# Kernel tuning notes

Hardware: AMD Instinct MI355X
Metric: run time of the kernel (lower is better)

## Reference

```python
import jax, jax.numpy as jnp
import numpy as np

B, S, H = 2, 256, 512
EPS = 1e-12  # TPLinker conditional LayerNorm default epsilon
NEG = -1e30  # finite stand-in for -inf in running max


def _cond_layer_norm(x, cond, Wg, Wb, gamma, beta):
    # TPLinker conditional LayerNorm: gamma/beta are modulated by a linear map of cond.
    g = gamma + cond @ Wg          # (..., H)
    b = beta + cond @ Wb           # (..., H)
    xc = x - jnp.mean(x, axis=-1, keepdims=True)
    inv = jax.lax.rsqrt(jnp.mean(xc * xc, axis=-1, keepdims=True) + EPS)
    return xc * inv * g + b


def setup_inputs() -> dict:
    key = jax.random.key(0)
    ks = jax.random.split(key, 6)
    return {
        "seq_hiddens": jax.random.normal(ks[0], (B, S, H), jnp.float32),
        "mask": jnp.ones((B, S), jnp.float32),
        "lamtha": jax.random.uniform(ks[1], (H,), jnp.float32),
        "Wg1": jax.random.normal(ks[2], (H, H), jnp.float32) * 0.02,
        "Wb1": jax.random.normal(ks[3], (H, H), jnp.float32) * 0.02,
        "g1": jnp.ones((H,), jnp.float32),
        "b1": jnp.zeros((H,), jnp.float32),
        "Wg2": jax.random.normal(ks[4], (H, H), jnp.float32) * 0.02,
        "Wb2": jax.random.normal(ks[5], (H, H), jnp.float32) * 0.02,
        "g2": jnp.ones((H,), jnp.float32),
        "b2": jnp.zeros((H,), jnp.float32),
    }


def reference(seq_hiddens, mask, lamtha, Wg1, Wb1, g1, b1, Wg2, Wb2, g2, b2):
    # mask additive penalty, broadcast over hidden (matches (1-mask)*-1000 expand)
    seq = seq_hiddens + ((1.0 - mask) * -1000.0)[:, :, None]  # (B,S,H)

    ii, jj = jnp.triu_indices(S)  # row-major pairs (i, j>=i), same order as the torch loop

    # window means over seq[i..j] via cumulative sums (replaces O(S^3) recomputation)
    csum = jnp.cumsum(seq, axis=1)                              # (B,S,H)
    lens = (jj - ii + 1).astype(seq.dtype)[None, :, None]
    mean_pairs = (csum[:, jj] - csum[:, ii] + seq[:, ii]) / lens  # (B,P,H)

    # window maxes over seq[i..j]: scan over j keeping running max per start i
    idx = jnp.arange(S)

    def step(state, j):
        sj = jnp.take(seq, j, axis=1)  # (B,H)
        new = jnp.where((idx <= j)[None, :, None],
                        jnp.maximum(state, sj[:, None, :]),
                        jnp.asarray(NEG, seq.dtype))
        return new, new

    _, Mall = jax.lax.scan(step, jnp.full((B, S, H), NEG, seq.dtype), idx)  # (S_j,B,S_i,H)
    max_pairs = Mall[jj, :, ii].transpose(1, 0, 2)  # (B,P,H)

    # mix pooling
    inner = lamtha * mean_pairs + (1.0 - lamtha) * max_pairs  # (B,P,H)

    visible = seq[:, jj]  # (B,P,H) token j
    repeat = seq[:, ii]   # (B,P,H) token i

    shaking = _cond_layer_norm(visible, repeat, Wg1, Wb1, g1, b1)
    return _cond_layer_norm(shaking, inner, Wg2, Wb2, g2, b2)
```

## Files before the change

### kernel.cpp

```cpp
#include <hip/hip_runtime.h>
#include <hip/hip_bf16.h>

typedef __hip_bfloat16 bf16;
typedef short short8 __attribute__((ext_vector_type(8)));
typedef float floatx4 __attribute__((ext_vector_type(4)));

#define S 256
#define H 512
#define P 32896
#define NROWS 65792
#define NEGF -1e30f
#define EPSF 1e-12f

#define OFF_LN1    2129920u
#define OFF_G1     3178496u
#define OFF_B1     4227072u
#define OFF_WCAT   5275648u
#define OFF_II     6324224u
#define OFF_JJ     6390016u
#define OFF_MU2    6455808u
#define OFF_INV2   6718976u
#define OFF_INNER  6982144u

__device__ __forceinline__ void gld_lds16(const void* g, void* l) {
    __builtin_amdgcn_global_load_lds(
        (const __attribute__((address_space(1))) void*)g,
        (__attribute__((address_space(3))) void*)l, 16, 0, 0);
}

__global__ __launch_bounds__(512) void fusedA_kernel(
    const float* __restrict__ x, const float* __restrict__ mask,
    float* __restrict__ ln1,
    const float* __restrict__ Wg2, const float* __restrict__ Wb2,
    bf16* __restrict__ wcatT,
    unsigned short* __restrict__ ii, unsigned short* __restrict__ jj) {
    __shared__ float part[8][8][2];
    __shared__ float rstat[8][2];
    if (blockIdx.x < 64) {
        int b = blockIdx.x >> 5, sc = blockIdx.x & 31, h = threadIdx.x;
        int wave = h >> 6, lane = h & 63;
        int s0 = sc * 8;
        float v[8];
#pragma unroll
        for (int t = 0; t < 8; ++t) {
            int s = s0 + t;
            v[t] = x[(size_t)(b * S + s) * H + h] + (1.0f - mask[b * S + s]) * (-1000.0f);
        }
#pragma unroll
        for (int t = 0; t < 8; ++t) {
            float s = v[t], q = v[t] * v[t];
            for (int o = 1; o < 64; o <<= 1) { s += __shfl_xor(s, o); q += __shfl_xor(q, o); }
            if (lane == 0) { part[wave][t][0] = s; part[wave][t][1] = q; }
        }
        __syncthreads();
        if (h < 16) {
            int row = h >> 1, st = h & 1;
            float a = 0.0f;
#pragma unroll
            for (int w = 0; w < 8; ++w) a += part[w][row][st];
            rstat[row][st] = a;
        }
        __syncthreads();
#pragma unroll
        for (int t = 0; t < 8; ++t) {
            float m = rstat[t][0] * (1.0f / 512.0f);
            float var = rstat[t][1] * (1.0f / 512.0f) - m * m;
            var = var < 0.0f ? 0.0f : var;
            float inv = rsqrtf(var + EPSF);
            ln1[(size_t)(b * S + s0 + t) * H + h] = (v[t] - m) * inv;
        }
    } else {
        int n = blockIdx.x - 64;
        if (n < 1024) {
            int k = threadIdx.x;
            int tt = n >> 7, c = n & 127;
            int h = tt * 64 + (c & 63);
            float v = (c < 64) ? Wg2[(size_t)k * H + h] : Wb2[(size_t)k * H + h];
            wcatT[(size_t)n * H + k] = __float2bfloat16(v);
        } else {
            int p = (n - 1024) * 512 + threadIdx.x;
            if (p >= P) return;
            float disc = 513.0f * 513.0f - 8.0f * (float)p;
            int i = (int)((513.0f - sqrtf(disc)) * 0.5f);
            i = i < 0 ? 0 : (i > S - 1 ? S - 1 : i);
            while (i > 0 && (i * S - i * (i - 1) / 2) > p) --i;
            while (i < S - 1 && ((i + 1) * S - (i + 1) * i / 2) <= p) ++i;
            int off = i * S - i * (i - 1) / 2;
            ii[p] = (unsigned short)i;
            jj[p] = (unsigned short)(i + (p - off));
        }
    }
}

__global__ __launch_bounds__(256) void g1b1_kernel(
    const float* __restrict__ x, const float* __restrict__ mask,
    const float* __restrict__ Wg1, const float* __restrict__ Wb1,
    const float* __restrict__ g1, const float* __restrict__ b1,
    float* __restrict__ G1, float* __restrict__ B1) {
    __shared__ float rowbuf[4][H];
    int grp = blockIdx.x;
    int mat = blockIdx.y;
    int tid = threadIdx.x;
    int h0 = tid, h1 = tid + 256;
    int r0 = grp * 4;
#pragma unroll
    for (int r = 0; r < 4; ++r) {
        int row = r0 + r;
        float add = (1.0f - mask[row]) * (-1000.0f);
        rowbuf[r][h0] = x[(size_t)row * H + h0] + add;
        rowbuf[r][h1] = x[(size_t)row * H + h1] + add;
    }
    __syncthreads();
    const float* W = mat ? Wb1 : Wg1;
    float acc[4][2] = {{0, 0}, {0, 0}, {0, 0}, {0, 0}};
#pragma unroll 2
    for (int k4 = 0; k4 < 128; ++k4) {
        float4 a0 = ((const float4*)rowbuf[0])[k4];
        float4 a1 = ((const float4*)rowbuf[1])[k4];
        float4 a2 = ((const float4*)rowbuf[2])[k4];
        float4 a3 = ((const float4*)rowbuf[3])[k4];
        float w00 = W[(size_t)(k4 * 4 + 0) * H + h0], w01 = W[(size_t)(k4 * 4 + 0) * H + h1];
        float w10 = W[(size_t)(k4 * 4 + 1) * H + h0], w11 = W[(size_t)(k4 * 4 + 1) * H + h1];
        float w20 = W[(size_t)(k4 * 4 + 2) * H + h0], w21 = W[(size_t)(k4 * 4 + 2) * H + h1];
        float w30 = W[(size_t)(k4 * 4 + 3) * H + h0], w31 = W[(size_t)(k4 * 4 + 3) * H + h1];
        acc[0][0] += a0.x * w00 + a0.y * w10 + a0.z * w20 + a0.w * w30;
        acc[0][1] += a0.x * w01 + a0.y * w11 + a0.z * w21 + a0.w * w31;
        acc[1][0] += a1.x * w00 + a1.y * w10 + a1.z * w20 + a1.w * w30;
        acc[1][1] += a1.x * w01 + a1.y * w11 + a1.z * w21 + a1.w * w31;
        acc[2][0] += a2.x * w00 + a2.y * w10 + a2.z * w20 + a2.w * w30;
        acc[2][1] += a2.x * w01 + a2.y * w11 + a2.z * w21 + a2.w * w31;
        acc[3][0] += a3.x * w00 + a3.y * w10 + a3.z * w20 + a3.w * w30;
        acc[3][1] += a3.x * w01 + a3.y * w11 + a3.z * w21 + a3.w * w31;
    }
    float bias0 = (mat ? b1 : g1)[h0];
    float bias1 = (mat ? b1 : g1)[h1];
    float* dst = mat ? B1 : G1;
#pragma unroll
    for (int r = 0; r < 4; ++r) {
        dst[(size_t)(r0 + r) * H + h0] = acc[r][0] + bias0;
        dst[(size_t)(r0 + r) * H + h1] = acc[r][1] + bias1;
    }
}

__global__ __launch_bounds__(256) void innerstats_kernel(
    const float* __restrict__ x, const float* __restrict__ mask,
    const float* __restrict__ lamtha,
    const float* __restrict__ ln1, const float* __restrict__ G1,
    const float* __restrict__ B1,
    bf16* __restrict__ inner, float* __restrict__ mu2, float* __restrict__ inv2) {
    __shared__ float maskadd[256];
    int id = blockIdx.x;
    int kind = id & 1, sub = id >> 1;
    int t = sub & 255, b = sub >> 8;
    int i = b ? (255 - t) : t;
    int tid = threadIdx.x;
    int off = i * S - i * (i - 1) / 2;

    if (kind == 0) {
        int h2 = tid;
        maskadd[tid] = (1.0f - mask[b * S + tid]) * (-1000.0f);
        __syncthreads();
        float2 lam = ((const float2*)lamtha)[h2];
        float2 oml = {1.0f - lam.x, 1.0f - lam.y};
        const float2* xb = (const float2*)(x + (size_t)b * S * H);
        float2 mrun = {NEGF, NEGF};
        float2 srun = {0.0f, 0.0f};
        size_t base = (size_t)b * P + (size_t)off;
        __hip_bfloat162* dst = (__hip_bfloat162*)inner;
        int j = i;
#define INNER_STEP(xx, jx)                                                 \
    {                                                                      \
        float ma = maskadd[jx];                                            \
        float vx = xx.x + ma, vy = xx.y + ma;                              \
        srun.x += vx;                                                      \
        srun.y += vy;                                                      \
        mrun.x = fmaxf(mrun.x, vx);                                        \
        mrun.y = fmaxf(mrun.y, vy);                                        \
        float rl = 1.0f / (float)((jx) - i + 1);                           \
        float mx = srun.x * rl;                                            \
        float my = srun.y * rl;                                            \
        __hip_bfloat162 o;                                                 \
        o.x = __float2bfloat16(lam.x * mx + oml.x * mrun.x);               \
        o.y = __float2bfloat16(lam.y * my + oml.y * mrun.y);               \
        dst[(base + (size_t)((jx) - i)) * 256 + h2] = o;                   \
    }
        for (; j + 4 <= S; j += 4) {
            float2 x0 = xb[(j + 0) * 256 + h2];
            float2 x1 = xb[(j + 1) * 256 + h2];
            float2 x2 = xb[(j + 2) * 256 + h2];
            float2 x3 = xb[(j + 3) * 256 + h2];
            INNER_STEP(x0, j + 0)
            INNER_STEP(x1, j + 1)
            INNER_STEP(x2, j + 2)
            INNER_STEP(x3, j + 3)
        }
        for (; j < S; ++j) {
            float2 xv = xb[j * 256 + h2];
            INNER_STEP(xv, j)
        }
#undef INNER_STEP
    } else {
        int wave = tid >> 6, lane = tid & 63;
        const float4* gp = (const float4*)(G1 + (size_t)(b * S + i) * H);
        const float4* bp = (const float4*)(B1 + (size_t)(b * S + i) * H);
        float4 ga = gp[lane * 2], gb = gp[lane * 2 + 1];
        float4 ba = bp[lane * 2], bb = bp[lane * 2 + 1];
        for (int j = i + wave; j < S; j += 4) {
            const float4* lp = (const float4*)(ln1 + (size_t)(b * S + j) * H);
            float4 a0 = lp[lane * 2], a1 = lp[lane * 2 + 1];
            float v0 = a0.x * ga.x + ba.x, v1 = a0.y * ga.y + ba.y;
            float v2 = a0.z * ga.z + ba.z, v3 = a0.w * ga.w + ba.w;
            float v4 = a1.x * gb.x + bb.x, v5 = a1.y * gb.y + bb.y;
            float v6 = a1.z * gb.z + bb.z, v7 = a1.w * gb.w + bb.w;
            float sum = ((v0 + v1) + (v2 + v3)) + ((v4 + v5) + (v6 + v7));
            float ss = ((v0 * v0 + v1 * v1) + (v2 * v2 + v3 * v3)) +
                       ((v4 * v4 + v5 * v5) + (v6 * v6 + v7 * v7));
            for (int o = 1; o < 64; o <<= 1) { sum += __shfl_xor(sum, o); ss += __shfl_xor(ss, o); }
            if (lane == 0) {
                int r = b * P + off + (j - i);
                float m = sum * (1.0f / 512.0f);
                float var = ss * (1.0f / 512.0f) - m * m;
                var = var < 0.0f ? 0.0f : var;
                mu2[r] = m;
                inv2[r] = rsqrtf(var + EPSF);
            }
        }
    }
}

__global__ __launch_bounds__(256, 2) void gemm_kernel(
    const bf16* __restrict__ inner, const bf16* __restrict__ wcatT,
    const float* __restrict__ g2, const float* __restrict__ b2,
    const float* __restrict__ ln1, const float* __restrict__ G1, const float* __restrict__ B1,
    const unsigned short* __restrict__ ii, const unsigned short* __restrict__ jj,
    const float* __restrict__ mu2, const float* __restrict__ inv2,
    float* __restrict__ out) {
    extern __shared__ __align__(16) char smem[];

    const int tid = threadIdx.x;
    const int wave = tid >> 6, lane = tid & 63;
    const int q = lane >> 4, l15 = lane & 15;
    const int wm = wave & 1, wn = wave >> 1;

    const int id = blockIdx.x;
    int rb, t;
    if (id < 4096) { rb = (id >> 6) * 8 + (id & 7); t = (id >> 3) & 7; }
    else           { int w = id - 4096; rb = 512 + (w & 1); t = w >> 1; }
    const int R0 = rb * 128;

    const int srow = tid >> 3;
    const int sx8 = ((tid & 7) ^ (srow & 7)) * 8;
    const bf16* const Ag = inner + (size_t)(R0 + srow) * H + sx8;
    const bf16* const Bg = wcatT + (size_t)(t * 128 + srow) * H + sx8;

    char* const A0 = smem;
    char* const B0 = smem + 16384;
    char* const A1 = smem + 32768;
    char* const B1s = smem + 49152;

    floatx4 acc[4][4];
#pragma unroll
    for (int a = 0; a < 4; ++a)
#pragma unroll
        for (int c = 0; c < 4; ++c) acc[a][c] = (floatx4){0.f, 0.f, 0.f, 0.f};

    auto STAGE = [&](int kt, char* Ad, char* Bd) {
#pragma unroll
        for (int i2 = 0; i2 < 4; ++i2)
            gld_lds16(Ag + (size_t)i2 * 32 * H + kt * 64, Ad + i2 * 4096 + wave * 1024);
#pragma unroll
        for (int i2 = 0; i2 < 4; ++i2)
            gld_lds16(Bg + (size_t)i2 * 32 * H + kt * 64, Bd + i2 * 4096 + wave * 1024);
    };

    STAGE(0, A0, B0);
    STAGE(1, A1, B1s);
    asm volatile("s_waitcnt vmcnt(8)" ::: "memory");
    asm volatile("s_barrier" ::: "memory");

#pragma unroll
    for (int kt = 0; kt < 8; ++kt) {
        char* const As = (kt & 1) ? A1 : A0;
        char* const Bs = (kt & 1) ? B1s : B0;

        short8 bfr[4][2], af[4][2];
#pragma unroll
        for (int ks = 0; ks < 2; ++ks) {
#pragma unroll
            for (int fn = 0; fn < 4; ++fn) {
                int nr = (fn < 2 ? wn * 32 + fn * 16 : 64 + wn * 32 + (fn - 2) * 16) + l15;
                bfr[fn][ks] = *(const short8*)(Bs + nr * 128 + (((ks * 4 + q) ^ (l15 & 7)) << 4));
            }
#pragma unroll
            for (int fm = 0; fm < 4; ++fm) {
                int mr = wm * 64 + fm * 16 + l15;
                af[fm][ks] = *(const short8*)(As + mr * 128 + (((ks * 4 + q) ^ (l15 & 7)) << 4));
            }
        }

        __builtin_amdgcn_s_setprio(1);
#pragma unroll
        for (int fm = 0; fm < 4; ++fm)
#pragma unroll
            for (int fn = 0; fn < 4; ++fn)
                acc[fm][fn] = __builtin_amdgcn_mfma_f32_16x16x32_bf16(af[fm][0], bfr[fn][0], acc[fm][fn], 0, 0, 0);
        __builtin_amdgcn_s_setprio(0);

        if (kt < 6) {
            asm volatile("s_waitcnt lgkmcnt(0)" ::: "memory");
            asm volatile("s_barrier" ::: "memory");
            STAGE(kt + 2, As, Bs);
        }

        __builtin_amdgcn_s_setprio(1);
#pragma unroll
        for (int fm = 0; fm < 4; ++fm)
#pragma unroll
            for (int fn = 0; fn < 4; ++fn)
                acc[fm][fn] = __builtin_amdgcn_mfma_f32_16x16x32_bf16(af[fm][1], bfr[fn][1], acc[fm][fn], 0, 0, 0);
        __builtin_amdgcn_s_setprio(0);

        if (kt < 6) {
            asm volatile("s_waitcnt vmcnt(8)" ::: "memory");
            asm volatile("s_barrier" ::: "memory");
        } else if (kt == 6) {
            asm volatile("s_waitcnt vmcnt(0)" ::: "memory");
            asm volatile("s_barrier" ::: "memory");
        }
    }

    float g2v[2], b2v[2];
#pragma unroll
    for (int fg = 0; fg < 2; ++fg) {
        int h = t * 64 + wn * 32 + fg * 16 + l15;
        g2v[fg] = g2[h];
        b2v[fg] = b2[h];
    }
#pragma unroll
    for (int fm = 0; fm < 4; ++fm) {
#pragma unroll
        for (int r = 0; r < 4; ++r) {
            int m = wm * 64 + fm * 16 + q * 4 + r;
            int rg = R0 + m;
            int b = (rg >= P) ? 1 : 0;
            int p = rg - b * P;
            int i = ii[p], j = jj[p];
            float mu = mu2[rg], iv = inv2[rg];
            const float* lp = ln1 + (size_t)(b * S + j) * H + t * 64 + wn * 32;
            const float* gp = G1 + (size_t)(b * S + i) * H + t * 64 + wn * 32;
            const float* bp = B1 + (size_t)(b * S + i) * H + t * 64 + wn * 32;
            float* op = out + (size_t)rg * H + t * 64 + wn * 32;
#pragma unroll
            for (int fg = 0; fg < 2; ++fg) {
                int c = fg * 16 + l15;
                float s = (lp[c] * gp[c] + bp[c] - mu) * iv;
                float G2v = acc[fm][fg][r] + g2v[fg];
                float B2v = acc[fm][fg + 2][r] + b2v[fg];
                op[c] = s * G2v + B2v;
            }
        }
    }
}

extern "C" void kernel_launch(void* const* d_in, const int* in_sizes, int n_in,
                              void* d_out, int out_size, void* d_ws, size_t ws_size,
                              hipStream_t stream) {
    const float* x = (const float*)d_in[0];
    const float* mask = (const float*)d_in[1];
    const float* lamtha = (const float*)d_in[2];
    const float* Wg1 = (const float*)d_in[3];
    const float* Wb1 = (const float*)d_in[4];
    const float* g1 = (const float*)d_in[5];
    const float* b1 = (const float*)d_in[6];
    const float* Wg2 = (const float*)d_in[7];
    const float* Wb2 = (const float*)d_in[8];
    const float* g2 = (const float*)d_in[9];
    const float* b2 = (const float*)d_in[10];
    float* out = (float*)d_out;

    char* ws = (char*)d_ws;
    float* ln1 = (float*)(ws + OFF_LN1);
    float* G1 = (float*)(ws + OFF_G1);
    float* B1 = (float*)(ws + OFF_B1);
    bf16* wcatT = (bf16*)(ws + OFF_WCAT);
    unsigned short* iiA = (unsigned short*)(ws + OFF_II);
    unsigned short* jjA = (unsigned short*)(ws + OFF_JJ);
    float* mu2 = (float*)(ws + OFF_MU2);
    float* inv2 = (float*)(ws + OFF_INV2);
    bf16* inner = (bf16*)(ws + OFF_INNER);

    static bool attr_set = false;
    if (!attr_set) {
        hipFuncSetAttribute((const void*)gemm_kernel,
                            hipFuncAttributeMaxDynamicSharedMemorySize, 65536);
        attr_set = true;
    }

    hipLaunchKernelGGL(fusedA_kernel, dim3(1153), dim3(512), 0, stream,
                       x, mask, ln1, Wg2, Wb2, wcatT, iiA, jjA);
    hipLaunchKernelGGL(g1b1_kernel, dim3(128, 2), dim3(256), 0, stream,
                       x, mask, Wg1, Wb1, g1, b1, G1, B1);
    hipLaunchKernelGGL(innerstats_kernel, dim3(1024), dim3(256), 0, stream,
                       x, mask, lamtha, ln1, G1, B1, inner, mu2, inv2);
    hipLaunchKernelGGL(gemm_kernel, dim3(4112), dim3(256), 65536, stream,
                       inner, wcatT, g2, b2, ln1, G1, B1, iiA, jjA, mu2, inv2, out);
}
```

Measured before the change: 301.5 us.

## Regroup preprocessing kernels by dependency to cut launch count from four to three

The inner-pooling producer, the G1/B1 matvec, the LN1 row normalisation, the weight transpose and the index tables all become independent block ranges of one pre-kernel. The stats pass that needs ln1/G1/B1 moves to its own kernel, so one launch is removed and the independent work can run concurrently. The inner loop also reads 1/len from a shared-memory table and uses a packed bf16x2 conversion, and the matvec inner loop is unrolled over 8 k values. The risk is load imbalance inside the combined grid, since the heavy inner blocks sit alongside many light transpose blocks.

```diff
diff --git a/kernel.cpp b/kernel.cpp
--- a/kernel.cpp
+++ b/kernel.cpp
@@ -28,161 +28,51 @@
         (__attribute__((address_space(3))) void*)l, 16, 0, 0);
 }
 
-__global__ __launch_bounds__(512) void fusedA_kernel(
+__global__ __launch_bounds__(256) void pre_kernel(
     const float* __restrict__ x, const float* __restrict__ mask,
-    float* __restrict__ ln1,
-    const float* __restrict__ Wg2, const float* __restrict__ Wb2,
-    bf16* __restrict__ wcatT,
-    unsigned short* __restrict__ ii, unsigned short* __restrict__ jj) {
-    __shared__ float part[8][8][2];
-    __shared__ float rstat[8][2];
-    if (blockIdx.x < 64) {
-        int b = blockIdx.x >> 5, sc = blockIdx.x & 31, h = threadIdx.x;
-        int wave = h >> 6, lane = h & 63;
-        int s0 = sc * 8;
-        float v[8];
-#pragma unroll
-        for (int t = 0; t < 8; ++t) {
-            int s = s0 + t;
-            v[t] = x[(size_t)(b * S + s) * H + h] + (1.0f - mask[b * S + s]) * (-1000.0f);
-        }
-#pragma unroll
-        for (int t = 0; t < 8; ++t) {
-            float s = v[t], q = v[t] * v[t];
-            for (int o = 1; o < 64; o <<= 1) { s += __shfl_xor(s, o); q += __shfl_xor(q, o); }
-            if (lane == 0) { part[wave][t][0] = s; part[wave][t][1] = q; }
-        }
-        __syncthreads();
-        if (h < 16) {
-            int row = h >> 1, st = h & 1;
-            float a = 0.0f;
-#pragma unroll
-            for (int w = 0; w < 8; ++w) a += part[w][row][st];
-            rstat[row][st] = a;
-        }
-        __syncthreads();
-#pragma unroll
-        for (int t = 0; t < 8; ++t) {
-            float m = rstat[t][0] * (1.0f / 512.0f);
-            float var = rstat[t][1] * (1.0f / 512.0f) - m * m;
-            var = var < 0.0f ? 0.0f : var;
-            float inv = rsqrtf(var + EPSF);
-            ln1[(size_t)(b * S + s0 + t) * H + h] = (v[t] - m) * inv;
-        }
-    } else {
-        int n = blockIdx.x - 64;
-        if (n < 1024) {
-            int k = threadIdx.x;
-            int tt = n >> 7, c = n & 127;
-            int h = tt * 64 + (c & 63);
-            float v = (c < 64) ? Wg2[(size_t)k * H + h] : Wb2[(size_t)k * H + h];
-            wcatT[(size_t)n * H + k] = __float2bfloat16(v);
-        } else {
-            int p = (n - 1024) * 512 + threadIdx.x;
-            if (p >= P) return;
-            float disc = 513.0f * 513.0f - 8.0f * (float)p;
-            int i = (int)((513.0f - sqrtf(disc)) * 0.5f);
-            i = i < 0 ? 0 : (i > S - 1 ? S - 1 : i);
-            while (i > 0 && (i * S - i * (i - 1) / 2) > p) --i;
-            while (i < S - 1 && ((i + 1) * S - (i + 1) * i / 2) <= p) ++i;
-            int off = i * S - i * (i - 1) / 2;
-            ii[p] = (unsigned short)i;
-            jj[p] = (unsigned short)(i + (p - off));
-        }
-    }
-}
-
-__global__ __launch_bounds__(256) void g1b1_kernel(
-    const float* __restrict__ x, const float* __restrict__ mask,
+    const float* __restrict__ lamtha,
     const float* __restrict__ Wg1, const float* __restrict__ Wb1,
     const float* __restrict__ g1, const float* __restrict__ b1,
-    float* __restrict__ G1, float* __restrict__ B1) {
+    const float* __restrict__ Wg2, const float* __restrict__ Wb2,
+    float* __restrict__ ln1, float* __restrict__ G1, float* __restrict__ B1,
+    bf16* __restrict__ wcatT,
+    unsigned short* __restrict__ ii, unsigned short* __restrict__ jj,
+    bf16* __restrict__ inner) {
+    __shared__ float sh_a[256];
+    __shared__ float sh_b[256];
     __shared__ float rowbuf[4][H];
-    int grp = blockIdx.x;
-    int mat = blockIdx.y;
-    int tid = threadIdx.x;
-    int h0 = tid, h1 = tid + 256;
-    int r0 = grp * 4;
-#pragma unroll
-    for (int r = 0; r < 4; ++r) {
-        int row = r0 + r;
-        float add = (1.0f - mask[row]) * (-1000.0f);
-        rowbuf[r][h0] = x[(size_t)row * H + h0] + add;
-        rowbuf[r][h1] = x[(size_t)row * H + h1] + add;
-    }
-    __syncthreads();
-    const float* W = mat ? Wb1 : Wg1;
-    float acc[4][2] = {{0, 0}, {0, 0}, {0, 0}, {0, 0}};
-#pragma unroll 2
-    for (int k4 = 0; k4 < 128; ++k4) {
-        float4 a0 = ((const float4*)rowbuf[0])[k4];
-        float4 a1 = ((const float4*)rowbuf[1])[k4];
-        float4 a2 = ((const float4*)rowbuf[2])[k4];
-        float4 a3 = ((const float4*)rowbuf[3])[k4];
-        float w00 = W[(size_t)(k4 * 4 + 0) * H + h0], w01 = W[(size_t)(k4 * 4 + 0) * H + h1];
-        float w10 = W[(size_t)(k4 * 4 + 1) * H + h0], w11 = W[(size_t)(k4 * 4 + 1) * H + h1];
-        float w20 = W[(size_t)(k4 * 4 + 2) * H + h0], w21 = W[(size_t)(k4 * 4 + 2) * H + h1];
-        float w30 = W[(size_t)(k4 * 4 + 3) * H + h0], w31 = W[(size_t)(k4 * 4 + 3) * H + h1];
-        acc[0][0] += a0.x * w00 + a0.y * w10 + a0.z * w20 + a0.w * w30;
-        acc[0][1] += a0.x * w01 + a0.y * w11 + a0.z * w21 + a0.w * w31;
-        acc[1][0] += a1.x * w00 + a1.y * w10 + a1.z * w20 + a1.w * w30;
-        acc[1][1] += a1.x * w01 + a1.y * w11 + a1.z * w21 + a1.w * w31;
-        acc[2][0] += a2.x * w00 + a2.y * w10 + a2.z * w20 + a2.w * w30;
-        acc[2][1] += a2.x * w01 + a2.y * w11 + a2.z * w21 + a2.w * w31;
-        acc[3][0] += a3.x * w00 + a3.y * w10 + a3.z * w20 + a3.w * w30;
-        acc[3][1] += a3.x * w01 + a3.y * w11 + a3.z * w21 + a3.w * w31;
-    }
-    float bias0 = (mat ? b1 : g1)[h0];
-    float bias1 = (mat ? b1 : g1)[h1];
-    float* dst = mat ? B1 : G1;
-#pragma unroll
-    for (int r = 0; r < 4; ++r) {
-        dst[(size_t)(r0 + r) * H + h0] = acc[r][0] + bias0;
-        dst[(size_t)(r0 + r) * H + h1] = acc[r][1] + bias1;
-    }
-}
-
-__global__ __launch_bounds__(256) void innerstats_kernel(
-    const float* __restrict__ x, const float* __restrict__ mask,
-    const float* __restrict__ lamtha,
-    const float* __restrict__ ln1, const float* __restrict__ G1,
-    const float* __restrict__ B1,
-    bf16* __restrict__ inner, float* __restrict__ mu2, float* __restrict__ inv2) {
-    __shared__ float maskadd[256];
-    int id = blockIdx.x;
-    int kind = id & 1, sub = id >> 1;
-    int t = sub & 255, b = sub >> 8;
-    int i = b ? (255 - t) : t;
-    int tid = threadIdx.x;
-    int off = i * S - i * (i - 1) / 2;
-
-    if (kind == 0) {
+    __shared__ float part[4][8][2];
+    __shared__ float rstat[8][2];
+    const int id = blockIdx.x, tid = threadIdx.x;
+
+    if (id < 512) {
+        int t = id & 255, b = id >> 8;
+        int i = b ? (255 - t) : t;
+        sh_a[tid] = (1.0f - mask[b * S + tid]) * (-1000.0f);
+        sh_b[tid] = 1.0f / (float)(tid + 1);
+        __syncthreads();
         int h2 = tid;
-        maskadd[tid] = (1.0f - mask[b * S + tid]) * (-1000.0f);
-        __syncthreads();
         float2 lam = ((const float2*)lamtha)[h2];
         float2 oml = {1.0f - lam.x, 1.0f - lam.y};
         const float2* xb = (const float2*)(x + (size_t)b * S * H);
         float2 mrun = {NEGF, NEGF};
         float2 srun = {0.0f, 0.0f};
-        size_t base = (size_t)b * P + (size_t)off;
+        size_t base = (size_t)b * P + (size_t)(i * S - i * (i - 1) / 2);
         __hip_bfloat162* dst = (__hip_bfloat162*)inner;
         int j = i;
 #define INNER_STEP(xx, jx)                                                 \
     {                                                                      \
-        float ma = maskadd[jx];                                            \
+        float ma = sh_a[jx];                                               \
         float vx = xx.x + ma, vy = xx.y + ma;                              \
         srun.x += vx;                                                      \
         srun.y += vy;                                                      \
         mrun.x = fmaxf(mrun.x, vx);                                        \
         mrun.y = fmaxf(mrun.y, vy);                                        \
-        float rl = 1.0f / (float)((jx) - i + 1);                           \
-        float mx = srun.x * rl;                                            \
-        float my = srun.y * rl;                                            \
-        __hip_bfloat162 o;                                                 \
-        o.x = __float2bfloat16(lam.x * mx + oml.x * mrun.x);               \
-        o.y = __float2bfloat16(lam.y * my + oml.y * mrun.y);               \
-        dst[(base + (size_t)((jx) - i)) * 256 + h2] = o;                   \
+        float rl = sh_b[(jx) - i];                                         \
+        float fx = lam.x * (srun.x * rl) + oml.x * mrun.x;                 \
+        float fy = lam.y * (srun.y * rl) + oml.y * mrun.y;                 \
+        dst[(base + (size_t)((jx) - i)) * 256 + h2] =                      \
+            __float22bfloat162_rn(make_float2(fx, fy));                    \
     }
         for (; j + 4 <= S; j += 4) {
             float2 x0 = xb[(j + 0) * 256 + h2];
@@ -199,31 +89,145 @@
             INNER_STEP(xv, j)
         }
 #undef INNER_STEP
+    } else if (id < 768) {
+        int sub = id - 512;
+        int grp = sub >> 1, mat = sub & 1;
+        int h0 = tid, h1 = tid + 256;
+        int r0 = grp * 4;
+#pragma unroll
+        for (int r = 0; r < 4; ++r) {
+            int row = r0 + r;
+            float add = (1.0f - mask[row]) * (-1000.0f);
+            rowbuf[r][h0] = x[(size_t)row * H + h0] + add;
+            rowbuf[r][h1] = x[(size_t)row * H + h1] + add;
+        }
+        __syncthreads();
+        const float* W = mat ? Wb1 : Wg1;
+        float acc[4][2] = {{0, 0}, {0, 0}, {0, 0}, {0, 0}};
+        for (int k8 = 0; k8 < 64; ++k8) {
+            float4 ra[4][2];
+#pragma unroll
+            for (int r = 0; r < 4; ++r) {
+                ra[r][0] = ((const float4*)rowbuf[r])[k8 * 2];
+                ra[r][1] = ((const float4*)rowbuf[r])[k8 * 2 + 1];
+            }
+            float w0[8], w1[8];
+#pragma unroll
+            for (int kk = 0; kk < 8; ++kk) {
+                w0[kk] = W[(size_t)(k8 * 8 + kk) * H + h0];
+                w1[kk] = W[(size_t)(k8 * 8 + kk) * H + h1];
+            }
+#pragma unroll
+            for (int r = 0; r < 4; ++r) {
+                acc[r][0] += ra[r][0].x * w0[0] + ra[r][0].y * w0[1] +
+                             ra[r][0].z * w0[2] + ra[r][0].w * w0[3] +
+                             ra[r][1].x * w0[4] + ra[r][1].y * w0[5] +
+                             ra[r][1].z * w0[6] + ra[r][1].w * w0[7];
+                acc[r][1] += ra[r][0].x * w1[0] + ra[r][0].y * w1[1] +
+                             ra[r][0].z * w1[2] + ra[r][0].w * w1[3] +
+                             ra[r][1].x * w1[4] + ra[r][1].y * w1[5] +
+                             ra[r][1].z * w1[6] + ra[r][1].w * w1[7];
+            }
+        }
+        float bias0 = (mat ? b1 : g1)[h0];
+        float bias1 = (mat ? b1 : g1)[h1];
+        float* dst = mat ? B1 : G1;
+#pragma unroll
+        for (int r = 0; r < 4; ++r) {
+            dst[(size_t)(r0 + r) * H + h0] = acc[r][0] + bias0;
+            dst[(size_t)(r0 + r) * H + h1] = acc[r][1] + bias1;
+        }
+    } else if (id < 832) {
+        int blk = id - 768;
+        int b = blk >> 5, sc = blk & 31;
+        int s0 = sc * 8;
+        int wave = tid >> 6, lane = tid & 63;
+        int h0 = tid, h1 = tid + 256;
+        float v0[8], v1[8];
+#pragma unroll
+        for (int t = 0; t < 8; ++t) {
+            int row = b * S + s0 + t;
+            float add = (1.0f - mask[row]) * (-1000.0f);
+            v0[t] = x[(size_t)row * H + h0] + add;
+            v1[t] = x[(size_t)row * H + h1] + add;
+        }
+#pragma unroll
+        for (int t = 0; t < 8; ++t) {
+            float s = v0[t] + v1[t];
+            float q = v0[t] * v0[t] + v1[t] * v1[t];
+            for (int o = 1; o < 64; o <<= 1) { s += __shfl_xor(s, o); q += __shfl_xor(q, o); }
+            if (lane == 0) { part[wave][t][0] = s; part[wave][t][1] = q; }
+        }
+        __syncthreads();
+        if (tid < 16) {
+            int row = tid >> 1, st = tid & 1;
+            rstat[row][st] = part[0][row][st] + part[1][row][st] +
+                             part[2][row][st] + part[3][row][st];
+        }
+        __syncthreads();
+#pragma unroll
+        for (int t = 0; t < 8; ++t) {
+            float m = rstat[t][0] * (1.0f / 512.0f);
+            float var = rstat[t][1] * (1.0f / 512.0f) - m * m;
+            var = var < 0.0f ? 0.0f : var;
+            float inv = rsqrtf(var + EPSF);
+            int row = b * S + s0 + t;
+            ln1[(size_t)row * H + h0] = (v0[t] - m) * inv;
+            ln1[(size_t)row * H + h1] = (v1[t] - m) * inv;
+        }
+    } else if (id < 1856) {
+        int n = id - 832;
+        int tt = n >> 7, c = n & 127;
+        int h = tt * 64 + (c & 63);
+        const float* Wsrc = (c < 64) ? Wg2 : Wb2;
+        int k0 = tid, k1 = tid + 256;
+        wcatT[(size_t)n * H + k0] = __float2bfloat16(Wsrc[(size_t)k0 * H + h]);
+        wcatT[(size_t)n * H + k1] = __float2bfloat16(Wsrc[(size_t)k1 * H + h]);
     } else {
-        int wave = tid >> 6, lane = tid & 63;
-        const float4* gp = (const float4*)(G1 + (size_t)(b * S + i) * H);
-        const float4* bp = (const float4*)(B1 + (size_t)(b * S + i) * H);
-        float4 ga = gp[lane * 2], gb = gp[lane * 2 + 1];
-        float4 ba = bp[lane * 2], bb = bp[lane * 2 + 1];
-        for (int j = i + wave; j < S; j += 4) {
-            const float4* lp = (const float4*)(ln1 + (size_t)(b * S + j) * H);
-            float4 a0 = lp[lane * 2], a1 = lp[lane * 2 + 1];
-            float v0 = a0.x * ga.x + ba.x, v1 = a0.y * ga.y + ba.y;
-            float v2 = a0.z * ga.z + ba.z, v3 = a0.w * ga.w + ba.w;
-            float v4 = a1.x * gb.x + bb.x, v5 = a1.y * gb.y + bb.y;
-            float v6 = a1.z * gb.z + bb.z, v7 = a1.w * gb.w + bb.w;
-            float sum = ((v0 + v1) + (v2 + v3)) + ((v4 + v5) + (v6 + v7));
-            float ss = ((v0 * v0 + v1 * v1) + (v2 * v2 + v3 * v3)) +
-                       ((v4 * v4 + v5 * v5) + (v6 * v6 + v7 * v7));
-            for (int o = 1; o < 64; o <<= 1) { sum += __shfl_xor(sum, o); ss += __shfl_xor(ss, o); }
-            if (lane == 0) {
-                int r = b * P + off + (j - i);
-                float m = sum * (1.0f / 512.0f);
-                float var = ss * (1.0f / 512.0f) - m * m;
-                var = var < 0.0f ? 0.0f : var;
-                mu2[r] = m;
-                inv2[r] = rsqrtf(var + EPSF);
-            }
+        int p = (id - 1856) * 256 + tid;
+        if (p >= P) return;
+        float disc = 513.0f * 513.0f - 8.0f * (float)p;
+        int i = (int)((513.0f - sqrtf(disc)) * 0.5f);
+        i = i < 0 ? 0 : (i > S - 1 ? S - 1 : i);
+        while (i > 0 && (i * S - i * (i - 1) / 2) > p) --i;
+        while (i < S - 1 && ((i + 1) * S - (i + 1) * i / 2) <= p) ++i;
+        int off = i * S - i * (i - 1) / 2;
+        ii[p] = (unsigned short)i;
+        jj[p] = (unsigned short)(i + (p - off));
+    }
+}
+
+__global__ __launch_bounds__(256) void stats_kernel(
+    const float* __restrict__ ln1, const float* __restrict__ G1,
+    const float* __restrict__ B1,
+    float* __restrict__ mu2, float* __restrict__ inv2) {
+    int id = blockIdx.x;
+    int t = id & 255, b = id >> 8;
+    int i = b ? (255 - t) : t;
+    int tid = threadIdx.x, wave = tid >> 6, lane = tid & 63;
+    int off = i * S - i * (i - 1) / 2;
+    const float4* gp = (const float4*)(G1 + (size_t)(b * S + i) * H);
+    const float4* bp = (const float4*)(B1 + (size_t)(b * S + i) * H);
+    float4 ga = gp[lane * 2], gb = gp[lane * 2 + 1];
+    float4 ba = bp[lane * 2], bb = bp[lane * 2 + 1];
+    for (int j = i + wave; j < S; j += 4) {
+        const float4* lp = (const float4*)(ln1 + (size_t)(b * S + j) * H);
+        float4 a0 = lp[lane * 2], a1 = lp[lane * 2 + 1];
+        float v0 = a0.x * ga.x + ba.x, v1 = a0.y * ga.y + ba.y;
+        float v2 = a0.z * ga.z + ba.z, v3 = a0.w * ga.w + ba.w;
+        float v4 = a1.x * gb.x + bb.x, v5 = a1.y * gb.y + bb.y;
+        float v6 = a1.z * gb.z + bb.z, v7 = a1.w * gb.w + bb.w;
+        float sum = ((v0 + v1) + (v2 + v3)) + ((v4 + v5) + (v6 + v7));
+        float ss = ((v0 * v0 + v1 * v1) + (v2 * v2 + v3 * v3)) +
+                   ((v4 * v4 + v5 * v5) + (v6 * v6 + v7 * v7));
+        for (int o = 1; o < 64; o <<= 1) { sum += __shfl_xor(sum, o); ss += __shfl_xor(ss, o); }
+        if (lane == 0) {
+            int r = b * P + off + (j - i);
+            float m = sum * (1.0f / 512.0f);
+            float var = ss * (1.0f / 512.0f) - m * m;
+            var = var < 0.0f ? 0.0f : var;
+            mu2[r] = m;
+            inv2[r] = rsqrtf(var + EPSF);
         }
     }
 }
@@ -396,12 +400,11 @@
         attr_set = true;
     }
 
-    hipLaunchKernelGGL(fusedA_kernel, dim3(1153), dim3(512), 0, stream,
-                       x, mask, ln1, Wg2, Wb2, wcatT, iiA, jjA);
-    hipLaunchKernelGGL(g1b1_kernel, dim3(128, 2), dim3(256), 0, stream,
-                       x, mask, Wg1, Wb1, g1, b1, G1, B1);
-    hipLaunchKernelGGL(innerstats_kernel, dim3(1024), dim3(256), 0, stream,
-                       x, mask, lamtha, ln1, G1, B1, inner, mu2, inv2);
+    hipLaunchKernelGGL(pre_kernel, dim3(1985), dim3(256), 0, stream,
+                       x, mask, lamtha, Wg1, Wb1, g1, b1, Wg2, Wb2,
+                       ln1, G1, B1, wcatT, iiA, jjA, inner);
+    hipLaunchKernelGGL(stats_kernel, dim3(512), dim3(256), 0, stream,
+                       ln1, G1, B1, mu2, inv2);
     hipLaunchKernelGGL(gemm_kernel, dim3(4112), dim3(256), 65536, stream,
                        inner, wcatT, g2, b2, ln1, G1, B1, iiA, jjA, mu2, inv2, out);
 }
```

Measured after the change: 307.6 us. +2.0%, slower.

## Retile GEMM to 256-row blocks with K=32 stages and regroup weight layout

Applied to the files above, without the earlier changes.

The main GEMM now uses 256x128 output tiles instead of 128x128, with half-width K stages (32 elements) and a new swizzled LDS layout. The weight transpose is reordered so each wave's G/B columns sit together. The aim is to halve the number of blocks and re-reads of the weight tile, raising MFMA work per LDS load. It doubles accumulator registers (8x4 floatx4), which risks occupancy under launch_bounds(256,2). Smaller edits unroll the g1b1 K loop by 8 and replace the per-step reciprocal in innerstats with an LDS lookup table plus a packed bf16 convert.

```diff
diff --git a/kernel.cpp b/kernel.cpp
--- a/kernel.cpp
+++ b/kernel.cpp
@@ -73,10 +73,11 @@
         int n = blockIdx.x - 64;
         if (n < 1024) {
             int k = threadIdx.x;
-            int tt = n >> 7, c = n & 127;
-            int h = tt * 64 + (c & 63);
-            float v = (c < 64) ? Wg2[(size_t)k * H + h] : Wb2[(size_t)k * H + h];
-            wcatT[(size_t)n * H + k] = __float2bfloat16(v);
+            int tt = n >> 7, u = n & 127;
+            int wnn = u >> 6, v = u & 63;
+            int h = tt * 64 + wnn * 32 + (v & 31);
+            float val = (v < 32) ? Wg2[(size_t)k * H + h] : Wb2[(size_t)k * H + h];
+            wcatT[(size_t)n * H + k] = __float2bfloat16(val);
         } else {
             int p = (n - 1024) * 512 + threadIdx.x;
             if (p >= P) return;
@@ -113,24 +114,30 @@
     __syncthreads();
     const float* W = mat ? Wb1 : Wg1;
     float acc[4][2] = {{0, 0}, {0, 0}, {0, 0}, {0, 0}};
-#pragma unroll 2
-    for (int k4 = 0; k4 < 128; ++k4) {
-        float4 a0 = ((const float4*)rowbuf[0])[k4];
-        float4 a1 = ((const float4*)rowbuf[1])[k4];
-        float4 a2 = ((const float4*)rowbuf[2])[k4];
-        float4 a3 = ((const float4*)rowbuf[3])[k4];
-        float w00 = W[(size_t)(k4 * 4 + 0) * H + h0], w01 = W[(size_t)(k4 * 4 + 0) * H + h1];
-        float w10 = W[(size_t)(k4 * 4 + 1) * H + h0], w11 = W[(size_t)(k4 * 4 + 1) * H + h1];
-        float w20 = W[(size_t)(k4 * 4 + 2) * H + h0], w21 = W[(size_t)(k4 * 4 + 2) * H + h1];
-        float w30 = W[(size_t)(k4 * 4 + 3) * H + h0], w31 = W[(size_t)(k4 * 4 + 3) * H + h1];
-        acc[0][0] += a0.x * w00 + a0.y * w10 + a0.z * w20 + a0.w * w30;
-        acc[0][1] += a0.x * w01 + a0.y * w11 + a0.z * w21 + a0.w * w31;
-        acc[1][0] += a1.x * w00 + a1.y * w10 + a1.z * w20 + a1.w * w30;
-        acc[1][1] += a1.x * w01 + a1.y * w11 + a1.z * w21 + a1.w * w31;
-        acc[2][0] += a2.x * w00 + a2.y * w10 + a2.z * w20 + a2.w * w30;
-        acc[2][1] += a2.x * w01 + a2.y * w11 + a2.z * w21 + a2.w * w31;
-        acc[3][0] += a3.x * w00 + a3.y * w10 + a3.z * w20 + a3.w * w30;
-        acc[3][1] += a3.x * w01 + a3.y * w11 + a3.z * w21 + a3.w * w31;
+    for (int k8 = 0; k8 < 64; ++k8) {
+        float4 ra[4][2];
+#pragma unroll
+        for (int r = 0; r < 4; ++r) {
+            ra[r][0] = ((const float4*)rowbuf[r])[k8 * 2];
+            ra[r][1] = ((const float4*)rowbuf[r])[k8 * 2 + 1];
+        }
+        float w0[8], w1[8];
+#pragma unroll
+        for (int kk = 0; kk < 8; ++kk) {
+            w0[kk] = W[(size_t)(k8 * 8 + kk) * H + h0];
+            w1[kk] = W[(size_t)(k8 * 8 + kk) * H + h1];
+        }
+#pragma unroll
+        for (int r = 0; r < 4; ++r) {
+            acc[r][0] += ra[r][0].x * w0[0] + ra[r][0].y * w0[1] +
+                         ra[r][0].z * w0[2] + ra[r][0].w * w0[3] +
+                         ra[r][1].x * w0[4] + ra[r][1].y * w0[5] +
+                         ra[r][1].z * w0[6] + ra[r][1].w * w0[7];
+            acc[r][1] += ra[r][0].x * w1[0] + ra[r][0].y * w1[1] +
+                         ra[r][0].z * w1[2] + ra[r][0].w * w1[3] +
+                         ra[r][1].x * w1[4] + ra[r][1].y * w1[5] +
+                         ra[r][1].z * w1[6] + ra[r][1].w * w1[7];
+        }
     }
     float bias0 = (mat ? b1 : g1)[h0];
     float bias1 = (mat ? b1 : g1)[h1];
@@ -148,7 +155,8 @@
     const float* __restrict__ ln1, const float* __restrict__ G1,
     const float* __restrict__ B1,
     bf16* __restrict__ inner, float* __restrict__ mu2, float* __restrict__ inv2) {
-    __shared__ float maskadd[256];
+    __shared__ float sh_a[256];
+    __shared__ float sh_b[256];
     int id = blockIdx.x;
     int kind = id & 1, sub = id >> 1;
     int t = sub & 255, b = sub >> 8;
@@ -158,7 +166,8 @@
 
     if (kind == 0) {
         int h2 = tid;
-        maskadd[tid] = (1.0f - mask[b * S + tid]) * (-1000.0f);
+        sh_a[tid] = (1.0f - mask[b * S + tid]) * (-1000.0f);
+        sh_b[tid] = 1.0f / (float)(tid + 1);
         __syncthreads();
         float2 lam = ((const float2*)lamtha)[h2];
         float2 oml = {1.0f - lam.x, 1.0f - lam.y};
@@ -170,19 +179,17 @@
         int j = i;
 #define INNER_STEP(xx, jx)                                                 \
     {                                                                      \
-        float ma = maskadd[jx];                                            \
+        float ma = sh_a[jx];                                               \
         float vx = xx.x + ma, vy = xx.y + ma;                              \
         srun.x += vx;                                                      \
         srun.y += vy;                                                      \
         mrun.x = fmaxf(mrun.x, vx);                                        \
         mrun.y = fmaxf(mrun.y, vy);                                        \
-        float rl = 1.0f / (float)((jx) - i + 1);                           \
-        float mx = srun.x * rl;                                            \
-        float my = srun.y * rl;                                            \
-        __hip_bfloat162 o;                                                 \
-        o.x = __float2bfloat16(lam.x * mx + oml.x * mrun.x);               \
-        o.y = __float2bfloat16(lam.y * my + oml.y * mrun.y);               \
-        dst[(base + (size_t)((jx) - i)) * 256 + h2] = o;                   \
+        float rl = sh_b[(jx) - i];                                         \
+        float fx = lam.x * (srun.x * rl) + oml.x * mrun.x;                 \
+        float fy = lam.y * (srun.y * rl) + oml.y * mrun.y;                 \
+        dst[(base + (size_t)((jx) - i)) * 256 + h2] =                      \
+            __float22bfloat162_rn(make_float2(fx, fy));                    \
     }
         for (; j + 4 <= S; j += 4) {
             float2 x0 = xb[(j + 0) * 256 + h2];
@@ -244,69 +251,76 @@
 
     const int id = blockIdx.x;
     int rb, t;
-    if (id < 4096) { rb = (id >> 6) * 8 + (id & 7); t = (id >> 3) & 7; }
-    else           { int w = id - 4096; rb = 512 + (w & 1); t = w >> 1; }
-    const int R0 = rb * 128;
-
-    const int srow = tid >> 3;
-    const int sx8 = ((tid & 7) ^ (srow & 7)) * 8;
-    const bf16* const Ag = inner + (size_t)(R0 + srow) * H + sx8;
-    const bf16* const Bg = wcatT + (size_t)(t * 128 + srow) * H + sx8;
+    if (id < 2048) { rb = (id >> 6) * 8 + (id & 7); t = (id >> 3) & 7; }
+    else           { rb = 256; t = id - 2048; }
+    const int R0 = rb * 256;
+
+    int arow[4], acq[4];
+#pragma unroll
+    for (int s2 = 0; s2 < 4; ++s2) {
+        int ci = s2 * 256 + tid;
+        int pr = ci >> 3, pc = ci & 7, l = pc ^ (pr & 7);
+        arow[s2] = (pr << 1) | (l >> 2);
+        acq[s2] = l & 3;
+    }
+    const bf16* Asrc0 = inner + (size_t)(R0 + arow[0]) * H + acq[0] * 8;
+    const bf16* Asrc1 = inner + (size_t)(R0 + arow[1]) * H + acq[1] * 8;
+    const bf16* Asrc2 = inner + (size_t)(R0 + arow[2]) * H + acq[2] * 8;
+    const bf16* Asrc3 = inner + (size_t)(R0 + arow[3]) * H + acq[3] * 8;
+    const bf16* Bsrc0 = wcatT + (size_t)(t * 128 + arow[0]) * H + acq[0] * 8;
+    const bf16* Bsrc1 = wcatT + (size_t)(t * 128 + arow[1]) * H + acq[1] * 8;
 
     char* const A0 = smem;
     char* const B0 = smem + 16384;
-    char* const A1 = smem + 32768;
-    char* const B1s = smem + 49152;
-
-    floatx4 acc[4][4];
-#pragma unroll
-    for (int a = 0; a < 4; ++a)
+    char* const A1 = smem + 24576;
+    char* const B1s = smem + 40960;
+
+    const int prl = l15 >> 1;
+    const int apc = ((((l15 & 1) << 2) | q) ^ prl) << 4;
+    const int C = prl * 128 + apc;
+
+    floatx4 acc[8][4];
+#pragma unroll
+    for (int a = 0; a < 8; ++a)
 #pragma unroll
         for (int c = 0; c < 4; ++c) acc[a][c] = (floatx4){0.f, 0.f, 0.f, 0.f};
 
     auto STAGE = [&](int kt, char* Ad, char* Bd) {
-#pragma unroll
-        for (int i2 = 0; i2 < 4; ++i2)
-            gld_lds16(Ag + (size_t)i2 * 32 * H + kt * 64, Ad + i2 * 4096 + wave * 1024);
-#pragma unroll
-        for (int i2 = 0; i2 < 4; ++i2)
-            gld_lds16(Bg + (size_t)i2 * 32 * H + kt * 64, Bd + i2 * 4096 + wave * 1024);
+        gld_lds16(Asrc0 + kt * 32, Ad + 0 * 4096 + wave * 1024);
+        gld_lds16(Asrc1 + kt * 32, Ad + 1 * 4096 + wave * 1024);
+        gld_lds16(Asrc2 + kt * 32, Ad + 2 * 4096 + wave * 1024);
+        gld_lds16(Asrc3 + kt * 32, Ad + 3 * 4096 + wave * 1024);
+        gld_lds16(Bsrc0 + kt * 32, Bd + 0 * 4096 + wave * 1024);
+        gld_lds16(Bsrc1 + kt * 32, Bd + 1 * 4096 + wave * 1024);
     };
 
     STAGE(0, A0, B0);
     STAGE(1, A1, B1s);
-    asm volatile("s_waitcnt vmcnt(8)" ::: "memory");
+    asm volatile("s_waitcnt vmcnt(6)" ::: "memory");
     asm volatile("s_barrier" ::: "memory");
 
 #pragma unroll
-    for (int kt = 0; kt < 8; ++kt) {
+    for (int kt = 0; kt < 16; ++kt) {
         char* const As = (kt & 1) ? A1 : A0;
         char* const Bs = (kt & 1) ? B1s : B0;
 
-        short8 bfr[4][2], af[4][2];
-#pragma unroll
-        for (int ks = 0; ks < 2; ++ks) {
-#pragma unroll
-            for (int fn = 0; fn < 4; ++fn) {
-                int nr = (fn < 2 ? wn * 32 + fn * 16 : 64 + wn * 32 + (fn - 2) * 16) + l15;
-                bfr[fn][ks] = *(const short8*)(Bs + nr * 128 + (((ks * 4 + q) ^ (l15 & 7)) << 4));
-            }
-#pragma unroll
-            for (int fm = 0; fm < 4; ++fm) {
-                int mr = wm * 64 + fm * 16 + l15;
-                af[fm][ks] = *(const short8*)(As + mr * 128 + (((ks * 4 + q) ^ (l15 & 7)) << 4));
-            }
-        }
+        short8 af[8], bfr[4];
+#pragma unroll
+        for (int fn = 0; fn < 4; ++fn)
+            bfr[fn] = *(const short8*)(Bs + wn * 4096 + fn * 1024 + C);
+#pragma unroll
+        for (int fm = 0; fm < 8; ++fm)
+            af[fm] = *(const short8*)(As + wm * 8192 + fm * 1024 + C);
 
         __builtin_amdgcn_s_setprio(1);
 #pragma unroll
         for (int fm = 0; fm < 4; ++fm)
 #pragma unroll
             for (int fn = 0; fn < 4; ++fn)
-                acc[fm][fn] = __builtin_amdgcn_mfma_f32_16x16x32_bf16(af[fm][0], bfr[fn][0], acc[fm][fn], 0, 0, 0);
+                acc[fm][fn] = __builtin_amdgcn_mfma_f32_16x16x32_bf16(af[fm], bfr[fn], acc[fm][fn], 0, 0, 0);
         __builtin_amdgcn_s_setprio(0);
 
-        if (kt < 6) {
+        if (kt < 14) {
             asm volatile("s_waitcnt lgkmcnt(0)" ::: "memory");
             asm volatile("s_barrier" ::: "memory");
             STAGE(kt + 2, As, Bs);
@@ -314,16 +328,16 @@
 
         __builtin_amdgcn_s_setprio(1);
 #pragma unroll
-        for (int fm = 0; fm < 4; ++fm)
+        for (int fm = 4; fm < 8; ++fm)
 #pragma unroll
             for (int fn = 0; fn < 4; ++fn)
-                acc[fm][fn] = __builtin_amdgcn_mfma_f32_16x16x32_bf16(af[fm][1], bfr[fn][1], acc[fm][fn], 0, 0, 0);
+                acc[fm][fn] = __builtin_amdgcn_mfma_f32_16x16x32_bf16(af[fm], bfr[fn], acc[fm][fn], 0, 0, 0);
         __builtin_amdgcn_s_setprio(0);
 
-        if (kt < 6) {
-            asm volatile("s_waitcnt vmcnt(8)" ::: "memory");
+        if (kt < 14) {
+            asm volatile("s_waitcnt vmcnt(6)" ::: "memory");
             asm volatile("s_barrier" ::: "memory");
-        } else if (kt == 6) {
+        } else if (kt == 14) {
             asm volatile("s_waitcnt vmcnt(0)" ::: "memory");
             asm volatile("s_barrier" ::: "memory");
         }
@@ -337,10 +351,10 @@
         b2v[fg] = b2[h];
     }
 #pragma unroll
-    for (int fm = 0; fm < 4; ++fm) {
+    for (int fm = 0; fm < 8; ++fm) {
 #pragma unroll
         for (int r = 0; r < 4; ++r) {
-            int m = wm * 64 + fm * 16 + q * 4 + r;
+            int m = wm * 128 + fm * 16 + q * 4 + r;
             int rg = R0 + m;
             int b = (rg >= P) ? 1 : 0;
             int p = rg - b * P;
@@ -392,7 +406,7 @@
     static bool attr_set = false;
     if (!attr_set) {
         hipFuncSetAttribute((const void*)gemm_kernel,
-                            hipFuncAttributeMaxDynamicSharedMemorySize, 65536);
+                            hipFuncAttributeMaxDynamicSharedMemorySize, 49152);
         attr_set = true;
     }
 
@@ -402,6 +416,6 @@
                        x, mask, Wg1, Wb1, g1, b1, G1, B1);
     hipLaunchKernelGGL(innerstats_kernel, dim3(1024), dim3(256), 0, stream,
                        x, mask, lamtha, ln1, G1, B1, inner, mu2, inv2);
-    hipLaunchKernelGGL(gemm_kernel, dim3(4112), dim3(256), 65536, stream,
+    hipLaunchKernelGGL(gemm_kernel, dim3(2056), dim3(256), 49152, stream,
                        inner, wcatT, g2, b2, ln1, G1, B1, iiA, jjA, mu2, inv2, out);
 }
```

Result: no change. 306.9 us (+1.8%).
